# Kernel tuning notes

Measured on AMD Instinct MI355X. Metric: run time of the kernel, lower is better.

Reference implementation:

```python
import jax, jax.numpy as jnp
import numpy as np

NEG = jnp.float32(-1e30)  # max-plus identity (finite to keep grads clean)


def setup_inputs() -> dict:
    key = jax.random.key(0)
    k1, k2 = jax.random.split(key)
    B, Cin, H, W = 8, 64, 64, 64
    Cout, kH, kW = 64, 3, 3
    x = jax.random.normal(k1, (B, Cin, H, W), dtype=jnp.float32)
    weight = jax.random.normal(k2, (Cout, Cin, kH, kW), dtype=jnp.float32)
    return {"x": x, "weight": weight, "kernel_size": 3, "padding": 1}


def reference(x, weight, kernel_size, padding):
    # Max-plus correlation (tropical conv), stride 1:
    #   out[b,co,y,x] = max_{ci,i,j} ( x_pad[b,ci,y+i,x+j] + weight[co,ci,i,j] )
    kH = kW = int(kernel_size)
    padH = padW = int(padding)
    B, Cin, H, W = x.shape
    Cout = weight.shape[0]
    xp = jnp.pad(x, ((0, 0), (0, 0), (padH, padH), (padW, padW)),
                 constant_values=NEG)  # -inf-like padding: identity of max
    Ho = H + 2 * padH - kH + 1
    Wo = W + 2 * padW - kW + 1
    out = jnp.full((B, Cout, Ho, Wo), NEG, dtype=x.dtype)
    for i in range(kH):          # small fixed kernel loop (kH*kW taps)
        for j in range(kW):
            win = xp[:, :, i:i + Ho, j:j + Wo]            # [B,Ci,Ho,Wo]
            cand = win[:, None] + weight[None, :, :, i, j, None, None]
            out = jnp.maximum(out, cand.max(axis=2))      # reduce over Ci
    return out
```

## Files before the change

kernel.cpp:

```cpp
#include <hip/hip_runtime.h>

#define NEGV -1e30f

constexpr int Bn = 8, Ci = 64, Hn = 64, Wn = 64, Co = 64;
constexpr int WT_ELEMS = Ci * 9 * Co;

__global__ __launch_bounds__(256)
void wtrans_kernel(const float* __restrict__ wt, float* __restrict__ wT) {
    int idx = blockIdx.x * 256 + threadIdx.x;
    if (idx < WT_ELEMS) {
        int co = idx & 63;
        int k  = (idx >> 6) % 9;
        int ci = idx / 576;
        wT[idx] = wt[((size_t)co * Ci + ci) * 9 + k];
    }
}

__device__ __forceinline__ float vmax3(float a, float b, float c) {
    float d;
    asm("v_max3_f32 %0, %1, %2, %3" : "=v"(d) : "v"(a), "v"(b), "v"(c));
    return d;
}

__device__ __forceinline__ void read10(float* o, const float* __restrict__ p) {
    float4 a = *reinterpret_cast<const float4*>(p);
    float4 b = *reinterpret_cast<const float4*>(p + 4);
    float2 c = *reinterpret_cast<const float2*>(p + 8);
    o[0] = a.x; o[1] = a.y; o[2] = a.z; o[3] = a.w;
    o[4] = b.x; o[5] = b.y; o[6] = b.z; o[7] = b.w;
    o[8] = c.x; o[9] = c.y;
}

__device__ __forceinline__ void compute8(float* acc, const float* xu,
                                         const float* xc, const float* xd,
                                         const float* wv) {
#pragma unroll
    for (int j = 0; j < 8; j++) {
        float t0 = xu[j] + wv[0], t1 = xu[j + 1] + wv[1], t2 = xu[j + 2] + wv[2];
        float t3 = xc[j] + wv[3], t4 = xc[j + 1] + wv[4], t5 = xc[j + 2] + wv[5];
        float t6 = xd[j] + wv[6], t7 = xd[j + 1] + wv[7], t8 = xd[j + 2] + wv[8];
        float m0 = vmax3(t0, t1, t2);
        float m1 = vmax3(t3, t4, t5);
        float m2 = vmax3(t6, t7, t8);
        acc[j] = vmax3(acc[j], m0, m1);
        acc[j] = fmaxf(acc[j], m2);
    }
}

__global__ __launch_bounds__(256, 4)
void maxconv_main(const float* __restrict__ x, const float* __restrict__ wT,
                  float* __restrict__ out) {
    __shared__ __align__(16) float xs[Ci * 120];

    const int tid  = threadIdx.x;
    const int lane = tid & 63;
    const int wvid = tid >> 6;

    const int lg   = ((blockIdx.x & 7) << 7) | (blockIdx.x >> 3);
    const int b    = lg >> 7;
    const int rem  = lg & 127;
    const int h    = rem >> 1;
    const int half = rem & 1;
    const int w0h  = half << 5;

    {
        const int st     = (tid < 128) ? tid : tid - 128;
        const int cibase = (tid < 128) ? 0 : 32;
        if (st < 102) {
            const int r    = st / 34;
            const int s    = st - r * 34;
            const int grow = h - 1 + r;
            const int gcol = w0h - 1 + s;
            const bool valid = (grow >= 0) && (grow < Hn) && (gcol >= 0) && (gcol < Wn);
            const int cg   = valid ? grow : 0;
            const int cc   = valid ? gcol : 0;
            const float* gp = x + (((size_t)b * Ci + cibase) * Hn + cg) * Wn + cc;
            const int dst  = r * 40 + s;
#pragma unroll 1
            for (int c8 = 0; c8 < 32; c8 += 8) {
                float v[8];
#pragma unroll
                for (int i = 0; i < 8; i++)
                    v[i] = valid ? gp[(size_t)(c8 + i) * Hn * Wn] : NEGV;
#pragma unroll
                for (int i = 0; i < 8; i++)
                    xs[(cibase + c8 + i) * 120 + dst] = v[i];
            }
        }
    }
    __syncthreads();

    const int woff = wvid * 8;

    float acc[8];
#pragma unroll
    for (int j = 0; j < 8; j++) acc[j] = NEGV;

#pragma unroll 1
    for (int ci = 0; ci < Ci; ci += 2) {
        const float* wrow = wT + ci * 576;
        float wv[9];
#pragma unroll
        for (int k = 0; k < 9; k++) wv[k] = wrow[k * 64 + lane];
        float xu[10], xc[10], xd[10];
        const float* base0 = xs + ci * 120 + woff;
        read10(xu, base0); read10(xc, base0 + 40); read10(xd, base0 + 80);
        compute8(acc, xu, xc, xd, wv);

        const float* wrow2 = wrow + 576;
        float wv2[9];
#pragma unroll
        for (int k = 0; k < 9; k++) wv2[k] = wrow2[k * 64 + lane];
        const float* base1 = base0 + 120;
        read10(xu, base1); read10(xc, base1 + 40); read10(xd, base1 + 80);
        compute8(acc, xu, xc, xd, wv2);
    }

    float* po = out + (((size_t)b * Co + lane) * Hn + h) * Wn + w0h + woff;
    *reinterpret_cast<float4*>(po)     = make_float4(acc[0], acc[1], acc[2], acc[3]);
    *reinterpret_cast<float4*>(po + 4) = make_float4(acc[4], acc[5], acc[6], acc[7]);
}

extern "C" void kernel_launch(void* const* d_in, const int* in_sizes, int n_in,
                              void* d_out, int out_size, void* d_ws, size_t ws_size,
                              hipStream_t stream) {
    const float* x  = (const float*)d_in[0];
    const float* wt = (const float*)d_in[1];
    float* out = (float*)d_out;
    float* wT  = (float*)d_ws;

    wtrans_kernel<<<(WT_ELEMS + 255) / 256, 256, 0, stream>>>(wt, wT);

    maxconv_main<<<1024, 256, 0, stream>>>(x, wT, out);
}
```

Before: 114.8 us.

## Drop LDS staging and read input rows directly from global memory per wave

Removes the shared-memory tile fill and block barrier, so each wave loads its 3 input rows straight from global memory. The loads use wave-uniform addresses (readfirstlane), which lets them be served as scalar or broadcast loads. Image-border handling moves into templated variants for the top and bottom rows plus left and right edge flags. The cost is repeated global/L2 reads of overlapping rows across waves and blocks in place of a single cooperative stage.

```diff
diff --git a/kernel.cpp b/kernel.cpp
--- a/kernel.cpp
+++ b/kernel.cpp
@@ -4,6 +4,7 @@
 
 constexpr int Bn = 8, Ci = 64, Hn = 64, Wn = 64, Co = 64;
 constexpr int WT_ELEMS = Ci * 9 * Co;
+constexpr int HW = Hn * Wn;
 
 __global__ __launch_bounds__(256)
 void wtrans_kernel(const float* __restrict__ wt, float* __restrict__ wT) {
@@ -22,13 +23,16 @@
     return d;
 }
 
-__device__ __forceinline__ void read10(float* o, const float* __restrict__ p) {
-    float4 a = *reinterpret_cast<const float4*>(p);
-    float4 b = *reinterpret_cast<const float4*>(p + 4);
-    float2 c = *reinterpret_cast<const float2*>(p + 8);
-    o[0] = a.x; o[1] = a.y; o[2] = a.z; o[3] = a.w;
-    o[4] = b.x; o[5] = b.y; o[6] = b.z; o[7] = b.w;
-    o[8] = c.x; o[9] = c.y;
+__device__ __forceinline__ void rowload(float* o, const float* __restrict__ p,
+                                        int w0, bool eL, bool eR) {
+    float4 a = *reinterpret_cast<const float4*>(p + w0);
+    float4 c = *reinterpret_cast<const float4*>(p + w0 + 4);
+    float l = p[w0 - 1 + (eL ? 1 : 0)];
+    float r = p[w0 + 8 - (eR ? 1 : 0)];
+    o[0] = eL ? NEGV : l;
+    o[1] = a.x; o[2] = a.y; o[3] = a.z; o[4] = a.w;
+    o[5] = c.x; o[6] = c.y; o[7] = c.z; o[8] = c.w;
+    o[9] = eR ? NEGV : r;
 }
 
 __device__ __forceinline__ void compute8(float* acc, const float* xu,
@@ -47,50 +51,39 @@
     }
 }
 
-__global__ __launch_bounds__(256, 4)
-void maxconv_main(const float* __restrict__ x, const float* __restrict__ wT,
-                  float* __restrict__ out) {
-    __shared__ __align__(16) float xs[Ci * 120];
+template<int RE>
+__device__ __forceinline__ void body(float* acc, const float* __restrict__ pc,
+                                     const float* __restrict__ wp,
+                                     int w0, bool eL, bool eR) {
+    float wv[9];
+#pragma unroll
+    for (int k = 0; k < 9; k++) wv[k] = wp[k * 64];
 
-    const int tid  = threadIdx.x;
-    const int lane = tid & 63;
-    const int wvid = tid >> 6;
+    float xu[10], xc[10], xd[10];
+    rowload(xc, pc, w0, eL, eR);
+    if (RE != 1) rowload(xu, pc - Wn, w0, eL, eR);
+    else {
+#pragma unroll
+        for (int c = 0; c < 10; c++) xu[c] = NEGV;
+    }
+    if (RE != 2) rowload(xd, pc + Wn, w0, eL, eR);
+    else {
+#pragma unroll
+        for (int c = 0; c < 10; c++) xd[c] = NEGV;
+    }
+    compute8(acc, xu, xc, xd, wv);
+}
 
-    const int lg   = ((blockIdx.x & 7) << 7) | (blockIdx.x >> 3);
-    const int b    = lg >> 7;
-    const int rem  = lg & 127;
-    const int h    = rem >> 1;
-    const int half = rem & 1;
-    const int w0h  = half << 5;
+template<int RE>
+__device__ __forceinline__ void run_wave(const float* __restrict__ x,
+                                         const float* __restrict__ wT,
+                                         float* __restrict__ out,
+                                         int b, int h, int w0, int lane) {
+    const bool eL = (w0 == 0);
+    const bool eR = (w0 == Wn - 8);
 
-    {
-        const int st     = (tid < 128) ? tid : tid - 128;
-        const int cibase = (tid < 128) ? 0 : 32;
-        if (st < 102) {
-            const int r    = st / 34;
-            const int s    = st - r * 34;
-            const int grow = h - 1 + r;
-            const int gcol = w0h - 1 + s;
-            const bool valid = (grow >= 0) && (grow < Hn) && (gcol >= 0) && (gcol < Wn);
-            const int cg   = valid ? grow : 0;
-            const int cc   = valid ? gcol : 0;
-            const float* gp = x + (((size_t)b * Ci + cibase) * Hn + cg) * Wn + cc;
-            const int dst  = r * 40 + s;
-#pragma unroll 1
-            for (int c8 = 0; c8 < 32; c8 += 8) {
-                float v[8];
-#pragma unroll
-                for (int i = 0; i < 8; i++)
-                    v[i] = valid ? gp[(size_t)(c8 + i) * Hn * Wn] : NEGV;
-#pragma unroll
-                for (int i = 0; i < 8; i++)
-                    xs[(cibase + c8 + i) * 120 + dst] = v[i];
-            }
-        }
-    }
-    __syncthreads();
-
-    const int woff = wvid * 8;
+    const float* pc = x + (((size_t)b * Ci) * Hn + h) * Wn;
+    const float* wp = wT + lane;
 
     float acc[8];
 #pragma unroll
@@ -98,27 +91,31 @@
 
 #pragma unroll 1
     for (int ci = 0; ci < Ci; ci += 2) {
-        const float* wrow = wT + ci * 576;
-        float wv[9];
-#pragma unroll
-        for (int k = 0; k < 9; k++) wv[k] = wrow[k * 64 + lane];
-        float xu[10], xc[10], xd[10];
-        const float* base0 = xs + ci * 120 + woff;
-        read10(xu, base0); read10(xc, base0 + 40); read10(xd, base0 + 80);
-        compute8(acc, xu, xc, xd, wv);
-
-        const float* wrow2 = wrow + 576;
-        float wv2[9];
-#pragma unroll
-        for (int k = 0; k < 9; k++) wv2[k] = wrow2[k * 64 + lane];
-        const float* base1 = base0 + 120;
-        read10(xu, base1); read10(xc, base1 + 40); read10(xd, base1 + 80);
-        compute8(acc, xu, xc, xd, wv2);
+        body<RE>(acc, pc, wp, w0, eL, eR);  pc += HW;  wp += 576;
+        body<RE>(acc, pc, wp, w0, eL, eR);  pc += HW;  wp += 576;
     }
 
-    float* po = out + (((size_t)b * Co + lane) * Hn + h) * Wn + w0h + woff;
+    float* po = out + (((size_t)b * Co + lane) * Hn + h) * Wn + w0;
     *reinterpret_cast<float4*>(po)     = make_float4(acc[0], acc[1], acc[2], acc[3]);
     *reinterpret_cast<float4*>(po + 4) = make_float4(acc[4], acc[5], acc[6], acc[7]);
+}
+
+__global__ __launch_bounds__(256, 4)
+void maxconv_main(const float* __restrict__ x, const float* __restrict__ wT,
+                  float* __restrict__ out) {
+    const int lane = threadIdx.x & 63;
+    const int wvid = threadIdx.x >> 6;
+
+    const int lg   = ((blockIdx.x & 7) << 7) | (blockIdx.x >> 3);
+    const int b    = lg >> 7;
+    const int rem  = lg & 127;
+    const int h    = rem >> 1;
+    const int half = rem & 1;
+    const int w0 = __builtin_amdgcn_readfirstlane(half * 32 + wvid * 8);
+
+    if (h == 0)            run_wave<1>(x, wT, out, b, h, w0, lane);
+    else if (h == Hn - 1)  run_wave<2>(x, wT, out, b, h, w0, lane);
+    else                   run_wave<0>(x, wT, out, b, h, w0, lane);
 }
 
 extern "C" void kernel_launch(void* const* d_in, const int* in_sizes, int n_in,
```

After: 132.0 us. 1.15x slower.

## Split input-channel reduction across two wave groups with shared-memory max combine

Applied to the files above, without the earlier changes.

Doubles the block to 512 threads and has each pair of waves split the 64 input channels in half. Partial maxima are then combined through shared memory before the store, and the tile load is spread over four thread groups. The aim is more waves in flight and shorter per-thread loops to hide LDS and global latency. In exchange it adds two barriers, an LDS round trip and tighter register limits from the launch bounds.

```diff
diff --git a/kernel.cpp b/kernel.cpp
--- a/kernel.cpp
+++ b/kernel.cpp
@@ -4,6 +4,7 @@
 
 constexpr int Bn = 8, Ci = 64, Hn = 64, Wn = 64, Co = 64;
 constexpr int WT_ELEMS = Ci * 9 * Co;
+constexpr int HW = Hn * Wn;
 
 __global__ __launch_bounds__(256)
 void wtrans_kernel(const float* __restrict__ wt, float* __restrict__ wT) {
@@ -47,14 +48,14 @@
     }
 }
 
-__global__ __launch_bounds__(256, 4)
+__global__ __launch_bounds__(512, 8)
 void maxconv_main(const float* __restrict__ x, const float* __restrict__ wT,
                   float* __restrict__ out) {
     __shared__ __align__(16) float xs[Ci * 120];
 
     const int tid  = threadIdx.x;
     const int lane = tid & 63;
-    const int wvid = tid >> 6;
+    const int wid  = tid >> 6;
 
     const int lg   = ((blockIdx.x & 7) << 7) | (blockIdx.x >> 3);
     const int b    = lg >> 7;
@@ -64,8 +65,9 @@
     const int w0h  = half << 5;
 
     {
-        const int st     = (tid < 128) ? tid : tid - 128;
-        const int cibase = (tid < 128) ? 0 : 32;
+        const int q      = tid >> 7;
+        const int st     = tid & 127;
+        const int cibase = q * 16;
         if (st < 102) {
             const int r    = st / 34;
             const int s    = st - r * 34;
@@ -77,11 +79,11 @@
             const float* gp = x + (((size_t)b * Ci + cibase) * Hn + cg) * Wn + cc;
             const int dst  = r * 40 + s;
 #pragma unroll 1
-            for (int c8 = 0; c8 < 32; c8 += 8) {
+            for (int c8 = 0; c8 < 16; c8 += 8) {
                 float v[8];
 #pragma unroll
                 for (int i = 0; i < 8; i++)
-                    v[i] = valid ? gp[(size_t)(c8 + i) * Hn * Wn] : NEGV;
+                    v[i] = valid ? gp[(size_t)(c8 + i) * HW] : NEGV;
 #pragma unroll
                 for (int i = 0; i < 8; i++)
                     xs[(cibase + c8 + i) * 120 + dst] = v[i];
@@ -90,35 +92,56 @@
     }
     __syncthreads();
 
-    const int woff = wvid * 8;
+    const int quad   = wid >> 1;
+    const int cihalf = wid & 1;
+    const int woff   = quad * 8;
+
+    const float* wq = wT + (size_t)cihalf * 32 * 576 + lane;
+    const float* xq = xs + cihalf * 32 * 120 + woff;
 
     float acc[8];
 #pragma unroll
     for (int j = 0; j < 8; j++) acc[j] = NEGV;
 
 #pragma unroll 1
-    for (int ci = 0; ci < Ci; ci += 2) {
-        const float* wrow = wT + ci * 576;
+    for (int ci = 0; ci < 32; ci += 2) {
         float wv[9];
 #pragma unroll
-        for (int k = 0; k < 9; k++) wv[k] = wrow[k * 64 + lane];
+        for (int k = 0; k < 9; k++) wv[k] = wq[k * 64];
         float xu[10], xc[10], xd[10];
-        const float* base0 = xs + ci * 120 + woff;
-        read10(xu, base0); read10(xc, base0 + 40); read10(xd, base0 + 80);
+        read10(xu, xq); read10(xc, xq + 40); read10(xd, xq + 80);
         compute8(acc, xu, xc, xd, wv);
+        wq += 576; xq += 120;
 
-        const float* wrow2 = wrow + 576;
         float wv2[9];
 #pragma unroll
-        for (int k = 0; k < 9; k++) wv2[k] = wrow2[k * 64 + lane];
-        const float* base1 = base0 + 120;
-        read10(xu, base1); read10(xc, base1 + 40); read10(xd, base1 + 80);
-        compute8(acc, xu, xc, xd, wv2);
+        for (int k = 0; k < 9; k++) wv2[k] = wq[k * 64];
+        float yu[10], yc[10], yd[10];
+        read10(yu, xq); read10(yc, xq + 40); read10(yd, xq + 80);
+        compute8(acc, yu, yc, yd, wv2);
+        wq += 576; xq += 120;
     }
 
-    float* po = out + (((size_t)b * Co + lane) * Hn + h) * Wn + w0h + woff;
-    *reinterpret_cast<float4*>(po)     = make_float4(acc[0], acc[1], acc[2], acc[3]);
-    *reinterpret_cast<float4*>(po + 4) = make_float4(acc[4], acc[5], acc[6], acc[7]);
+    __syncthreads();
+    if (cihalf) {
+        float* ps = xs + quad * 512 + lane * 8;
+        *reinterpret_cast<float4*>(ps)     = make_float4(acc[0], acc[1], acc[2], acc[3]);
+        *reinterpret_cast<float4*>(ps + 4) = make_float4(acc[4], acc[5], acc[6], acc[7]);
+    }
+    __syncthreads();
+    if (!cihalf) {
+        const float* ps = xs + quad * 512 + lane * 8;
+        float4 o0 = *reinterpret_cast<const float4*>(ps);
+        float4 o1 = *reinterpret_cast<const float4*>(ps + 4);
+        acc[0] = fmaxf(acc[0], o0.x); acc[1] = fmaxf(acc[1], o0.y);
+        acc[2] = fmaxf(acc[2], o0.z); acc[3] = fmaxf(acc[3], o0.w);
+        acc[4] = fmaxf(acc[4], o1.x); acc[5] = fmaxf(acc[5], o1.y);
+        acc[6] = fmaxf(acc[6], o1.z); acc[7] = fmaxf(acc[7], o1.w);
+
+        float* po = out + (((size_t)b * Co + lane) * Hn + h) * Wn + w0h + woff;
+        *reinterpret_cast<float4*>(po)     = make_float4(acc[0], acc[1], acc[2], acc[3]);
+        *reinterpret_cast<float4*>(po + 4) = make_float4(acc[4], acc[5], acc[6], acc[7]);
+    }
 }
 
 extern "C" void kernel_launch(void* const* d_in, const int* in_sizes, int n_in,
@@ -131,5 +154,5 @@
 
     wtrans_kernel<<<(WT_ELEMS + 255) / 256, 256, 0, stream>>>(wt, wT);
 
-    maxconv_main<<<1024, 256, 0, stream>>>(x, wT, out);
+    maxconv_main<<<1024, 512, 0, stream>>>(x, wT, out);
 }
```

New measurement: 113.2 us. Within noise of the previous version (-1.4%).
